# Performance work log

Hardware: AMD Instinct MI355X
Metric: run time of the kernel (lower is better)

The kernel has to match this reference:

```python
import jax, jax.numpy as jnp
import numpy as np

N = 100000
E = 1600000
H = 128
M = 256
L = 6
G = 512          # number of graphs in the batch
A = 95           # num_atom_types
EXTRA = 3        # input_dim - 1
EPS = 1e-5


def swish(x):
    return x * jax.nn.sigmoid(x)


def setup_inputs() -> dict:
    key = jax.random.key(0)
    ks = jax.random.split(key, 16)
    z = jax.random.randint(ks[0], (N, 1), 0, A).astype(jnp.float32)
    extra = jax.random.normal(ks[1], (N, EXTRA), dtype=jnp.float32)
    x = jnp.concatenate([z, extra], axis=1)                     # [N, 4]
    edge_index = jax.random.randint(ks[2], (2, E), 0, N)        # [2, E]
    batch = jnp.sort(jax.random.randint(ks[3], (N,), 0, G))     # [N]
    s = 0.02
    z_embed = jax.random.normal(ks[4], (A, H), dtype=jnp.float32) * s
    extra_w = jax.random.normal(ks[5], (H, EXTRA), dtype=jnp.float32) * (1.0 / np.sqrt(EXTRA))
    extra_b = jnp.zeros((H,), jnp.float32)
    conv_w = jax.random.normal(ks[6], (L, H, H), dtype=jnp.float32) * (1.0 / np.sqrt(H))
    conv_b = jnp.zeros((L, H), jnp.float32)
    gamma = jnp.ones((L, H), jnp.float32)
    beta = jnp.zeros((L, H), jnp.float32)
    mean_scale = jnp.ones((L, H), jnp.float32)
    mlp_w1 = jax.random.normal(ks[7], (L, M, H), dtype=jnp.float32) * (1.0 / np.sqrt(H))
    mlp_b1 = jnp.zeros((L, M), jnp.float32)
    mlp_w2 = jax.random.normal(ks[8], (L, H, M), dtype=jnp.float32) * (1.0 / np.sqrt(M))
    mlp_b2 = jnp.zeros((L, H), jnp.float32)
    return dict(x=x, edge_index=edge_index, batch=batch, z_embed=z_embed,
                extra_w=extra_w, extra_b=extra_b, conv_w=conv_w, conv_b=conv_b,
                gamma=gamma, beta=beta, mean_scale=mean_scale,
                mlp_w1=mlp_w1, mlp_b1=mlp_b1, mlp_w2=mlp_w2, mlp_b2=mlp_b2)


def gnn_forward(x, edge_index, batch, z_embed, extra_w, extra_b, conv_w, conv_b,
                gamma, beta, mean_scale, mlp_w1, mlp_b1, mlp_w2, mlp_b2):
    z = x[:, 0].astype(jnp.int32)
    h = z_embed[z] + x[:, 1:] @ extra_w.T + extra_b                 # [N, H]

    # GCN: add self loops, symmetric normalization (computed once; graph is static)
    loop = jnp.arange(N)
    src = jnp.concatenate([edge_index[0], loop])
    dst = jnp.concatenate([edge_index[1], loop])
    deg = jax.ops.segment_sum(jnp.ones_like(dst, jnp.float32), dst, num_segments=N)
    dinv = jnp.where(deg > 0, jax.lax.rsqrt(jnp.maximum(deg, 1.0)), 0.0)
    norm = (dinv[src] * dinv[dst])[:, None]                         # [E+N, 1]

    cnt = jax.ops.segment_sum(jnp.ones((N,), jnp.float32), batch, num_segments=G)[:, None]
    cnt = jnp.maximum(cnt, 1.0)

    for i in range(L):
        h_res = h
        # GCNConv
        xw = h @ conv_w[i].T
        agg = jax.ops.segment_sum(xw[src] * norm, dst, num_segments=N) + conv_b[i]
        # GraphNorm: gamma * (x - alpha*mean) / sqrt(var + eps) + beta, per graph
        mean = jax.ops.segment_sum(agg, batch, num_segments=G) / cnt   # [G, H]
        sub = agg - mean_scale[i] * mean[batch]
        var = jax.ops.segment_sum(sub * sub, batch, num_segments=G) / cnt
        hn = gamma[i] * sub * jax.lax.rsqrt(var[batch] + EPS) + beta[i]
        ha = swish(hn)
        # residual MLP
        h = swish(swish(ha @ mlp_w1[i].T + mlp_b1[i]) @ mlp_w2[i].T + mlp_b2[i]) + h_res
    return h


def reference(x, edge_index, batch, z_embed, extra_w, extra_b, conv_w, conv_b,
              gamma, beta, mean_scale, mlp_w1, mlp_b1, mlp_w2, mlp_b2):
    return gnn_forward(x, edge_index, batch, z_embed, extra_w, extra_b, conv_w, conv_b,
                       gamma, beta, mean_scale, mlp_w1, mlp_b1, mlp_w2, mlp_b2)
```

## Files before the change

kernel.cpp:

```cpp
#include <hip/hip_runtime.h>

#define NN 100000
#define EE 1600000
#define HH 128
#define MM 256
#define LL 6
#define GG 512
#define SCAN_NB ((NN + 1023) / 1024)

typedef __attribute__((ext_vector_type(8))) short short8;
typedef __attribute__((ext_vector_type(4))) float floatx4;

__device__ __forceinline__ float swishf(float v) {
    return v / (1.0f + __expf(-v));
}

__device__ __forceinline__ unsigned short f2bf(float f) {
    unsigned u = __builtin_bit_cast(unsigned, f);
    unsigned r = u + 0x7FFFu + ((u >> 16) & 1u);
    return (unsigned short)(r >> 16);
}

__device__ __forceinline__ float bf2f(unsigned short u) {
    return __builtin_bit_cast(float, (unsigned)u << 16);
}

__device__ __forceinline__ float2 bf2f2(unsigned u) {
    float2 r;
    r.x = __builtin_bit_cast(float, u << 16);
    r.y = __builtin_bit_cast(float, u & 0xFFFF0000u);
    return r;
}

__device__ __forceinline__ uint4 pack8(const float* o) {
    uint4 pk;
    pk.x = (unsigned)f2bf(o[0]) | ((unsigned)f2bf(o[1]) << 16);
    pk.y = (unsigned)f2bf(o[2]) | ((unsigned)f2bf(o[3]) << 16);
    pk.z = (unsigned)f2bf(o[4]) | ((unsigned)f2bf(o[5]) << 16);
    pk.w = (unsigned)f2bf(o[6]) | ((unsigned)f2bf(o[7]) << 16);
    return pk;
}

__global__ void k_embed(const float* __restrict__ x, const float* __restrict__ z_embed,
                        const float* __restrict__ ew, const float* __restrict__ eb,
                        unsigned short* __restrict__ hb) {
    int idx = blockIdx.x * blockDim.x + threadIdx.x;
    if (idx >= NN * 32) return;
    int n = idx >> 5;
    int c0 = (idx & 31) << 2;
    const float* xr = x + (size_t)n * 4;
    int z = (int)xr[0];
    float x1 = xr[1], x2 = xr[2], x3 = xr[3];
    const float* ze = z_embed + (size_t)z * HH + c0;
    float o[4];
#pragma unroll
    for (int j = 0; j < 4; ++j) {
        int c = c0 + j;
        o[j] = ze[j] + x1 * ew[c * 3 + 0] + x2 * ew[c * 3 + 1] + x3 * ew[c * 3 + 2] + eb[c];
    }
    uint2 p;
    p.x = (unsigned)f2bf(o[0]) | ((unsigned)f2bf(o[1]) << 16);
    p.y = (unsigned)f2bf(o[2]) | ((unsigned)f2bf(o[3]) << 16);
    *(uint2*)(hb + (size_t)n * HH + c0) = p;
}

__global__ void k_f2bf3(const float* __restrict__ s1, unsigned short* __restrict__ d1, int n1,
                        const float* __restrict__ s2, unsigned short* __restrict__ d2, int n2,
                        const float* __restrict__ s3, unsigned short* __restrict__ d3, int n3) {
    int i = blockIdx.x * blockDim.x + threadIdx.x;
    if (i < n1) {
        d1[i] = f2bf(s1[i]);
    } else if (i < n1 + n2) {
        d2[i - n1] = f2bf(s2[i - n1]);
    } else if (i < n1 + n2 + n3) {
        d3[i - n1 - n2] = f2bf(s3[i - n1 - n2]);
    }
}

__global__ __launch_bounds__(256) void k_degree_p(const int* __restrict__ dst,
                                                  int* __restrict__ deg) {
    int part = blockIdx.x & 7;
    int blk = blockIdx.x >> 3;
    int nb = gridDim.x >> 3;
    int lo = (int)((long long)part * NN / 8);
    int hi = (int)((long long)(part + 1) * NN / 8);
    for (int e = blk * 256 + threadIdx.x; e < EE; e += nb * 256) {
        int d = dst[e];
        if (d >= lo && d < hi) atomicAdd(&deg[d], 1);
    }
}

__global__ void k_dinv(const int* __restrict__ deg, float* __restrict__ dinv) {
    int n = blockIdx.x * blockDim.x + threadIdx.x;
    if (n < NN) dinv[n] = rsqrtf((float)(deg[n] + 1));
}

__global__ void k_scan1(const int* __restrict__ deg, int* __restrict__ bsum) {
    __shared__ int sd[256];
    int t = threadIdx.x;
    int base = blockIdx.x * 1024 + t * 4;
    int s = 0;
#pragma unroll
    for (int j = 0; j < 4; ++j) {
        int i = base + j;
        if (i < NN) s += deg[i];
    }
    sd[t] = s;
    __syncthreads();
    for (int off = 128; off > 0; off >>= 1) {
        if (t < off) sd[t] += sd[t + off];
        __syncthreads();
    }
    if (t == 0) bsum[blockIdx.x] = sd[0];
}

__global__ void k_scan2(const int* __restrict__ bsum, int* __restrict__ boff) {
    __shared__ int sd[128];
    int t = threadIdx.x;
    int v = (t < SCAN_NB) ? bsum[t] : 0;
    sd[t] = v;
    __syncthreads();
    for (int off = 1; off < 128; off <<= 1) {
        int u = (t >= off) ? sd[t - off] : 0;
        __syncthreads();
        sd[t] += u;
        __syncthreads();
    }
    boff[t] = sd[t] - v;
}

__global__ void k_scan3(const int* __restrict__ deg, const int* __restrict__ boff,
                        int* __restrict__ rowptr) {
    __shared__ int sd[256];
    int t = threadIdx.x;
    int base = blockIdx.x * 1024 + t * 4;
    int v[4];
    int s = 0;
#pragma unroll
    for (int j = 0; j < 4; ++j) {
        int i = base + j;
        v[j] = (i < NN) ? deg[i] : 0;
        s += v[j];
    }
    sd[t] = s;
    __syncthreads();
    for (int off = 1; off < 256; off <<= 1) {
        int u = (t >= off) ? sd[t - off] : 0;
        __syncthreads();
        sd[t] += u;
        __syncthreads();
    }
    int run = boff[blockIdx.x] + sd[t] - s;
#pragma unroll
    for (int j = 0; j < 4; ++j) {
        int i = base + j;
        if (i < NN) rowptr[i] = run;
        if (i == NN - 1) rowptr[NN] = run + v[j];
        run += v[j];
    }
}

__global__ __launch_bounds__(256) void k_fill_p(const int* __restrict__ ei,
                                                const int* __restrict__ rowptr,
                                                int* __restrict__ cursor,
                                                int* __restrict__ col) {
    int part = blockIdx.x & 7;
    int blk = blockIdx.x >> 3;
    int nb = gridDim.x >> 3;
    int lo = (int)((long long)part * NN / 8);
    int hi = (int)((long long)(part + 1) * NN / 8);
    for (int e = blk * 256 + threadIdx.x; e < EE; e += nb * 256) {
        int d = ei[EE + e];
        if (d >= lo && d < hi) {
            int p = atomicAdd(&cursor[d], 1);
            col[rowptr[d] + p] = ei[e];
        }
    }
}

__global__ void k_gptr(const int* __restrict__ batch, int* __restrict__ gptr) {
    int n = blockIdx.x * blockDim.x + threadIdx.x;
    if (n >= NN) return;
    int b = batch[n];
    int pb = (n == 0) ? -1 : batch[n - 1];
    for (int g = pb + 1; g <= b; ++g) gptr[g] = n;
    if (n == NN - 1) {
        for (int g = b + 1; g <= GG; ++g) gptr[g] = NN;
    }
}

__global__ __launch_bounds__(256) void k_conv(const unsigned short* __restrict__ A,
                                              const unsigned short* __restrict__ B,
                                              const float* __restrict__ dinv,
                                              unsigned short* __restrict__ Cb) {
    __shared__ unsigned short Bs[128][HH + 8];
    const int tid = threadIdx.x;
    const int wave = tid >> 6;
    const int lane = tid & 63;
    const int quad = lane >> 4;
    const int l16 = lane & 15;
    const int wr = (wave & 1) << 6;
    const int wc = (wave >> 1) << 6;
    const int rowBase = blockIdx.x * 128;

    for (int i = tid; i < 128 * (HH / 8); i += 256) {
        int r = i / (HH / 8);
        int kk = (i % (HH / 8)) * 8;
        int rho = (r & 64) | ((r & 3) << 4) | ((r >> 2) & 15);
        *(uint4*)(&Bs[rho][kk]) = *(const uint4*)(B + (size_t)r * HH + kk);
    }

    floatx4 acc[4][4];
    const floatx4 zed = {0.f, 0.f, 0.f, 0.f};
#pragma unroll
    for (int i = 0; i < 4; ++i)
#pragma unroll
        for (int j = 0; j < 4; ++j) acc[i][j] = zed;

    int ar[4];
#pragma unroll
    for (int i = 0; i < 4; ++i) {
        int r = rowBase + wr + (i << 4) + l16;
        ar[i] = r < NN ? r : NN - 1;
    }

    __syncthreads();

#pragma unroll
    for (int ks = 0; ks < HH / 32; ++ks) {
        int k = (ks << 5) + (quad << 3);
        short8 a[4], b[4];
#pragma unroll
        for (int i = 0; i < 4; ++i) a[i] = *(const short8*)(A + (size_t)ar[i] * HH + k);
#pragma unroll
        for (int j = 0; j < 4; ++j) b[j] = *(const short8*)(&Bs[wc + (j << 4) + l16][k]);
#pragma unroll
        for (int i = 0; i < 4; ++i)
#pragma unroll
            for (int j = 0; j < 4; ++j)
                acc[i][j] =
                    __builtin_amdgcn_mfma_f32_16x16x32_bf16(a[i], b[j], acc[i][j], 0, 0, 0);
    }

    const int c0 = wc + (l16 << 2);
#pragma unroll
    for (int i = 0; i < 4; ++i) {
        int rb = rowBase + wr + (i << 4) + (quad << 2);
#pragma unroll
        for (int reg = 0; reg < 4; ++reg) {
            int r = rb + reg;
            if (r < NN) {
                float dv = dinv[r];
                float o[4];
#pragma unroll
                for (int j = 0; j < 4; ++j) o[j] = acc[i][j][reg] * dv;
                uint2 pk;
                pk.x = (unsigned)f2bf(o[0]) | ((unsigned)f2bf(o[1]) << 16);
                pk.y = (unsigned)f2bf(o[2]) | ((unsigned)f2bf(o[3]) << 16);
                *(uint2*)(Cb + (size_t)r * HH + c0) = pk;
            }
        }
    }
}

__global__ __launch_bounds__(256) void k_mlp(const unsigned short* __restrict__ ha,
                                             const unsigned short* __restrict__ W1,
                                             const float* __restrict__ b1,
                                             const unsigned short* __restrict__ W2,
                                             const float* __restrict__ b2,
                                             unsigned short* __restrict__ hb,
                                             float* __restrict__ h_out, int writeF) {
    __shared__ unsigned short ts[64][MM + 8];
    const int tid = threadIdx.x;
    const int wave = tid >> 6;
    const int lane = tid & 63;
    const int quad = lane >> 4;
    const int l16 = lane & 15;
    const int wrh = (wave & 1) << 5;
    const int rowBase = blockIdx.x * 64;

    const int wch = (wave >> 1) << 7;
    floatx4 acc1[2][8];
    const floatx4 zed = {0.f, 0.f, 0.f, 0.f};
#pragma unroll
    for (int i = 0; i < 2; ++i)
#pragma unroll
        for (int j = 0; j < 8; ++j) acc1[i][j] = zed;

    int ar[2];
#pragma unroll
    for (int i = 0; i < 2; ++i) {
        int r = rowBase + wrh + (i << 4) + l16;
        ar[i] = r < NN ? r : NN - 1;
    }

#pragma unroll
    for (int ks = 0; ks < HH / 32; ++ks) {
        int k = (ks << 5) + (quad << 3);
        short8 a[2], b[8];
#pragma unroll
        for (int i = 0; i < 2; ++i) a[i] = *(const short8*)(ha + (size_t)ar[i] * HH + k);
#pragma unroll
        for (int j = 0; j < 8; ++j) {
            int pc = wch + (l16 << 3) + j;
            b[j] = *(const short8*)(W1 + (size_t)pc * HH + k);
        }
#pragma unroll
        for (int i = 0; i < 2; ++i)
#pragma unroll
            for (int j = 0; j < 8; ++j)
                acc1[i][j] =
                    __builtin_amdgcn_mfma_f32_16x16x32_bf16(a[i], b[j], acc1[i][j], 0, 0, 0);
    }

    const int c0a = wch + (l16 << 3);
    float b1v[8];
    {
        float4 u = *(const float4*)(b1 + c0a);
        float4 v = *(const float4*)(b1 + c0a + 4);
        b1v[0] = u.x; b1v[1] = u.y; b1v[2] = u.z; b1v[3] = u.w;
        b1v[4] = v.x; b1v[5] = v.y; b1v[6] = v.z; b1v[7] = v.w;
    }
#pragma unroll
    for (int i = 0; i < 2; ++i) {
#pragma unroll
        for (int reg = 0; reg < 4; ++reg) {
            int lr = wrh + (i << 4) + (quad << 2) + reg;
            float o[8];
#pragma unroll
            for (int j = 0; j < 8; ++j) o[j] = swishf(acc1[i][j][reg] + b1v[j]);
            *(uint4*)(&ts[lr][c0a]) = pack8(o);
        }
    }
    __syncthreads();

    const int wc2 = (wave >> 1) << 6;
    floatx4 acc2[2][4];
#pragma unroll
    for (int i = 0; i < 2; ++i)
#pragma unroll
        for (int j = 0; j < 4; ++j) acc2[i][j] = zed;

#pragma unroll
    for (int ks = 0; ks < MM / 32; ++ks) {
        int k = (ks << 5) + (quad << 3);
        short8 a[2], b[4];
#pragma unroll
        for (int i = 0; i < 2; ++i)
            a[i] = *(const short8*)(&ts[wrh + (i << 4) + l16][k]);
#pragma unroll
        for (int j = 0; j < 4; ++j) {
            int pc = wc2 + (l16 << 2) + j;
            b[j] = *(const short8*)(W2 + (size_t)pc * MM + k);
        }
#pragma unroll
        for (int i = 0; i < 2; ++i)
#pragma unroll
            for (int j = 0; j < 4; ++j)
                acc2[i][j] =
                    __builtin_amdgcn_mfma_f32_16x16x32_bf16(a[i], b[j], acc2[i][j], 0, 0, 0);
    }

    const int c0 = wc2 + (l16 << 2);
    float4 b2v = *(const float4*)(b2 + c0);
    float bv[4] = {b2v.x, b2v.y, b2v.z, b2v.w};
#pragma unroll
    for (int i = 0; i < 2; ++i) {
        int rb = rowBase + wrh + (i << 4) + (quad << 2);
#pragma unroll
        for (int reg = 0; reg < 4; ++reg) {
            int r = rb + reg;
            if (r < NN) {
                uint2 rv = *(const uint2*)(hb + (size_t)r * HH + c0);
                float2 r01 = bf2f2(rv.x), r23 = bf2f2(rv.y);
                float o[4];
                o[0] = swishf(acc2[i][0][reg] + bv[0]) + r01.x;
                o[1] = swishf(acc2[i][1][reg] + bv[1]) + r01.y;
                o[2] = swishf(acc2[i][2][reg] + bv[2]) + r23.x;
                o[3] = swishf(acc2[i][3][reg] + bv[3]) + r23.y;
                uint2 pk;
                pk.x = (unsigned)f2bf(o[0]) | ((unsigned)f2bf(o[1]) << 16);
                pk.y = (unsigned)f2bf(o[2]) | ((unsigned)f2bf(o[3]) << 16);
                *(uint2*)(hb + (size_t)r * HH + c0) = pk;
                if (writeF)
                    *(float4*)(h_out + (size_t)r * HH + c0) =
                        make_float4(o[0], o[1], o[2], o[3]);
            }
        }
    }
}

__global__ __launch_bounds__(256) void k_agg(const unsigned short* __restrict__ y,
                                             const int* __restrict__ rowptr,
                                             const int* __restrict__ col,
                                             const float* __restrict__ dinv,
                                             const float* __restrict__ cb,
                                             unsigned short* __restrict__ agg) {
    int w = threadIdx.x >> 6;
    int lane = threadIdx.x & 63;
    int d = blockIdx.x * 4 + w;
    if (d >= NN) return;
    int grp = lane >> 4;
    int l16 = lane & 15;
    const uint4* yv = (const uint4*)y;
    float acc[8];
#pragma unroll
    for (int j = 0; j < 8; ++j) acc[j] = 0.f;
    if (grp == 0) {
        uint4 v = yv[(size_t)d * 16 + l16];
        float2 p0 = bf2f2(v.x), p1 = bf2f2(v.y), p2 = bf2f2(v.z), p3 = bf2f2(v.w);
        acc[0] = p0.x; acc[1] = p0.y; acc[2] = p1.x; acc[3] = p1.y;
        acc[4] = p2.x; acc[5] = p2.y; acc[6] = p3.x; acc[7] = p3.y;
    }
    int beg = rowptr[d];
    int end = rowptr[d + 1];
    for (int e = beg + grp; e < end; e += 4) {
        int s = col[e];
        uint4 v = yv[(size_t)s * 16 + l16];
        float2 p0 = bf2f2(v.x), p1 = bf2f2(v.y), p2 = bf2f2(v.z), p3 = bf2f2(v.w);
        acc[0] += p0.x; acc[1] += p0.y; acc[2] += p1.x; acc[3] += p1.y;
        acc[4] += p2.x; acc[5] += p2.y; acc[6] += p3.x; acc[7] += p3.y;
    }
#pragma unroll
    for (int j = 0; j < 8; ++j) {
        acc[j] += __shfl_xor(acc[j], 16, 64);
        acc[j] += __shfl_xor(acc[j], 32, 64);
    }
    if (grp == 0) {
        float dv = dinv[d];
        float4 c0 = *(const float4*)(cb + l16 * 8);
        float4 c1 = *(const float4*)(cb + l16 * 8 + 4);
        float o[8];
        o[0] = acc[0] * dv + c0.x; o[1] = acc[1] * dv + c0.y;
        o[2] = acc[2] * dv + c0.z; o[3] = acc[3] * dv + c0.w;
        o[4] = acc[4] * dv + c1.x; o[5] = acc[5] * dv + c1.y;
        o[6] = acc[6] * dv + c1.z; o[7] = acc[7] * dv + c1.w;
        *(uint4*)(agg + (size_t)d * HH + l16 * 8) = pack8(o);
    }
}

__global__ __launch_bounds__(512) void k_stats(const unsigned short* __restrict__ agg,
                                               const int* __restrict__ gptr,
                                               const float* __restrict__ ms,
                                               float* __restrict__ gmean,
                                               float* __restrict__ grstd) {
    __shared__ float s1[512];
    __shared__ float s2[512];
    int g = blockIdx.x;
    int t = threadIdx.x;
    int c = t & 127;
    int part = t >> 7;
    int beg = gptr[g];
    int end = gptr[g + 1];
    float S1 = 0.f, S2 = 0.f;
    for (int n = beg + part; n < end; n += 4) {
        float v = bf2f(agg[(size_t)n * HH + c]);
        S1 += v;
        S2 += v * v;
    }
    s1[t] = S1;
    s2[t] = S2;
    __syncthreads();
    if (part == 0) {
        S1 = (s1[c] + s1[c + 128]) + (s1[c + 256] + s1[c + 384]);
        S2 = (s2[c] + s2[c + 128]) + (s2[c + 256] + s2[c + 384]);
        int cnt = end - beg;
        float inv = 1.0f / (float)(cnt > 0 ? cnt : 1);
        float m = S1 * inv;
        float msc = ms[c];
        float var = S2 * inv - msc * (2.0f - msc) * m * m;
        gmean[g * HH + c] = m;
        grstd[g * HH + c] = rsqrtf(var + 1e-5f);
    }
}

__global__ void k_normswish(const unsigned short* __restrict__ agg,
                            const int* __restrict__ batch, const float* __restrict__ gamma,
                            const float* __restrict__ beta, const float* __restrict__ ms,
                            const float* __restrict__ gmean, const float* __restrict__ grstd,
                            unsigned short* __restrict__ ha) {
    int idx = blockIdx.x * blockDim.x + threadIdx.x;
    if (idx >= NN * 32) return;
    int n = idx >> 5;
    int c0 = (idx & 31) << 2;
    int g = batch[n];
    uint2 ain = *(const uint2*)(agg + (size_t)n * HH + c0);
    float2 a01 = bf2f2(ain.x);
    float2 a23 = bf2f2(ain.y);
    float av[4] = {a01.x, a01.y, a23.x, a23.y};
    unsigned short o[4];
#pragma unroll
    for (int j = 0; j < 4; ++j) {
        int c = c0 + j;
        float sub = av[j] - ms[c] * gmean[g * HH + c];
        float hn = gamma[c] * sub * grstd[g * HH + c] + beta[c];
        o[j] = f2bf(swishf(hn));
    }
    uint2 p;
    p.x = (unsigned)o[0] | ((unsigned)o[1] << 16);
    p.y = (unsigned)o[2] | ((unsigned)o[3] << 16);
    *(uint2*)(ha + (size_t)n * HH + c0) = p;
}

extern "C" void kernel_launch(void* const* d_in, const int* in_sizes, int n_in,
                              void* d_out, int out_size, void* d_ws, size_t ws_size,
                              hipStream_t stream) {
    const float* x = (const float*)d_in[0];
    const int* ei = (const int*)d_in[1];
    const int* batch = (const int*)d_in[2];
    const float* z_embed = (const float*)d_in[3];
    const float* extra_w = (const float*)d_in[4];
    const float* extra_b = (const float*)d_in[5];
    const float* conv_w = (const float*)d_in[6];
    const float* conv_b = (const float*)d_in[7];
    const float* gamma = (const float*)d_in[8];
    const float* beta = (const float*)d_in[9];
    const float* mean_scale = (const float*)d_in[10];
    const float* mlp_w1 = (const float*)d_in[11];
    const float* mlp_b1 = (const float*)d_in[12];
    const float* mlp_w2 = (const float*)d_in[13];
    const float* mlp_b2 = (const float*)d_in[14];
    float* h_out = (float*)d_out;

    char* wsB = (char*)d_ws;
    size_t off = 0;
    auto alloc = [&](size_t bytes) -> void* {
        void* p = (void*)(wsB + off);
        off = (off + bytes + 255) & ~(size_t)255;
        return p;
    };
    float* dinv = (float*)alloc((size_t)NN * 4);
    int* deg = (int*)alloc((size_t)NN * 4);
    int* cursor = (int*)alloc((size_t)NN * 4);
    int* rowptr = (int*)alloc((size_t)(NN + 1) * 4);
    int* bsum = (int*)alloc(128 * 4);
    int* boff = (int*)alloc(128 * 4);
    int* col = (int*)alloc((size_t)EE * 4);
    int* gptr = (int*)alloc((size_t)(GG + 1) * 4);
    float* gmean = (float*)alloc((size_t)GG * HH * 4);
    float* grstd = (float*)alloc((size_t)GG * HH * 4);
    unsigned short* wb =
        (unsigned short*)alloc((size_t)(LL * (HH * HH + MM * HH + HH * MM)) * 2);
    unsigned short* cwb = wb;
    unsigned short* w1b = wb + (size_t)LL * HH * HH;
    unsigned short* w2b = w1b + (size_t)LL * MM * HH;
    unsigned short* hb = (unsigned short*)alloc((size_t)NN * HH * 2);
    unsigned short* ybuf = (unsigned short*)alloc((size_t)NN * HH * 2);
    unsigned short* aggb = (unsigned short*)alloc((size_t)NN * HH * 2);

    hipMemsetAsync(deg, 0, (size_t)NN * 4, stream);
    hipMemsetAsync(cursor, 0, (size_t)NN * 4, stream);

    k_embed<<<(NN * 32 + 255) / 256, 256, 0, stream>>>(x, z_embed, extra_w, extra_b, hb);
    {
        int n1 = LL * HH * HH, n2 = LL * MM * HH, n3 = LL * HH * MM;
        int nt = n1 + n2 + n3;
        k_f2bf3<<<(nt + 255) / 256, 256, 0, stream>>>(conv_w, cwb, n1, mlp_w1, w1b, n2,
                                                      mlp_w2, w2b, n3);
    }
    k_degree_p<<<1024, 256, 0, stream>>>(ei + EE, deg);
    k_dinv<<<(NN + 255) / 256, 256, 0, stream>>>(deg, dinv);
    k_scan1<<<SCAN_NB, 256, 0, stream>>>(deg, bsum);
    k_scan2<<<1, 128, 0, stream>>>(bsum, boff);
    k_scan3<<<SCAN_NB, 256, 0, stream>>>(deg, boff, rowptr);
    k_fill_p<<<1024, 256, 0, stream>>>(ei, rowptr, cursor, col);
    k_gptr<<<(NN + 255) / 256, 256, 0, stream>>>(batch, gptr);

    int gconv = (NN + 127) / 128;
    int gmlp = (NN + 63) / 64;
    for (int i = 0; i < LL; ++i) {
        k_conv<<<gconv, 256, 0, stream>>>(hb, cwb + (size_t)i * HH * HH, dinv, ybuf);
        k_agg<<<(NN + 3) / 4, 256, 0, stream>>>(ybuf, rowptr, col, dinv,
                                                conv_b + (size_t)i * HH, aggb);
        k_stats<<<GG, 512, 0, stream>>>(aggb, gptr, mean_scale + (size_t)i * HH, gmean, grstd);
        k_normswish<<<(NN * 32 + 255) / 256, 256, 0, stream>>>(
            aggb, batch, gamma + (size_t)i * HH, beta + (size_t)i * HH,
            mean_scale + (size_t)i * HH, gmean, grstd, ybuf);
        k_mlp<<<gmlp, 256, 0, stream>>>(ybuf, w1b + (size_t)i * MM * HH,
                                        mlp_b1 + (size_t)i * MM, w2b + (size_t)i * HH * MM,
                                        mlp_b2 + (size_t)i * HH, hb, h_out,
                                        i == LL - 1 ? 1 : 0);
    }
}
```

Before: 1.445 ms.

## Fuse GraphNorm-swish, residual MLP and next-layer conv GEMM into one kernel

The per-layer normswish, MLP and next layer's conv GEMM kernels are merged into a single kernel. k_stats now precomputes per-graph affine coefficients (scale and shift) so normalization becomes one FMA applied while loading the A operand. The MLP output is staged in shared memory and immediately multiplied by the next layer's conv weights, which avoids writing and re-reading the normalized activations and the hidden state in global memory. In exchange the fused kernel holds more registers and LDS, which may reduce occupancy, and the conv GEMM now uses 64-row tiles instead of 128.

Result: faster. 1.416 ms (-2.0%).

```diff
diff --git a/kernel.cpp b/kernel.cpp
--- a/kernel.cpp
+++ b/kernel.cpp
@@ -32,12 +32,25 @@
     return r;
 }
 
+__device__ __forceinline__ void unpack8(uint4 v, float* a) {
+    float2 p0 = bf2f2(v.x), p1 = bf2f2(v.y), p2 = bf2f2(v.z), p3 = bf2f2(v.w);
+    a[0] = p0.x; a[1] = p0.y; a[2] = p1.x; a[3] = p1.y;
+    a[4] = p2.x; a[5] = p2.y; a[6] = p3.x; a[7] = p3.y;
+}
+
 __device__ __forceinline__ uint4 pack8(const float* o) {
     uint4 pk;
     pk.x = (unsigned)f2bf(o[0]) | ((unsigned)f2bf(o[1]) << 16);
     pk.y = (unsigned)f2bf(o[2]) | ((unsigned)f2bf(o[3]) << 16);
     pk.z = (unsigned)f2bf(o[4]) | ((unsigned)f2bf(o[5]) << 16);
     pk.w = (unsigned)f2bf(o[6]) | ((unsigned)f2bf(o[7]) << 16);
+    return pk;
+}
+
+__device__ __forceinline__ uint2 pack4(const float* o) {
+    uint2 pk;
+    pk.x = (unsigned)f2bf(o[0]) | ((unsigned)f2bf(o[1]) << 16);
+    pk.y = (unsigned)f2bf(o[2]) | ((unsigned)f2bf(o[3]) << 16);
     return pk;
 }
 
@@ -58,10 +71,7 @@
         int c = c0 + j;
         o[j] = ze[j] + x1 * ew[c * 3 + 0] + x2 * ew[c * 3 + 1] + x3 * ew[c * 3 + 2] + eb[c];
     }
-    uint2 p;
-    p.x = (unsigned)f2bf(o[0]) | ((unsigned)f2bf(o[1]) << 16);
-    p.y = (unsigned)f2bf(o[2]) | ((unsigned)f2bf(o[3]) << 16);
-    *(uint2*)(hb + (size_t)n * HH + c0) = p;
+    *(uint2*)(hb + (size_t)n * HH + c0) = pack4(o);
 }
 
 __global__ void k_f2bf3(const float* __restrict__ s1, unsigned short* __restrict__ d1, int n1,
@@ -254,137 +264,7 @@
                 float o[4];
 #pragma unroll
                 for (int j = 0; j < 4; ++j) o[j] = acc[i][j][reg] * dv;
-                uint2 pk;
-                pk.x = (unsigned)f2bf(o[0]) | ((unsigned)f2bf(o[1]) << 16);
-                pk.y = (unsigned)f2bf(o[2]) | ((unsigned)f2bf(o[3]) << 16);
-                *(uint2*)(Cb + (size_t)r * HH + c0) = pk;
-            }
-        }
-    }
-}
-
-__global__ __launch_bounds__(256) void k_mlp(const unsigned short* __restrict__ ha,
-                                             const unsigned short* __restrict__ W1,
-                                             const float* __restrict__ b1,
-                                             const unsigned short* __restrict__ W2,
-                                             const float* __restrict__ b2,
-                                             unsigned short* __restrict__ hb,
-                                             float* __restrict__ h_out, int writeF) {
-    __shared__ unsigned short ts[64][MM + 8];
-    const int tid = threadIdx.x;
-    const int wave = tid >> 6;
-    const int lane = tid & 63;
-    const int quad = lane >> 4;
-    const int l16 = lane & 15;
-    const int wrh = (wave & 1) << 5;
-    const int rowBase = blockIdx.x * 64;
-
-    const int wch = (wave >> 1) << 7;
-    floatx4 acc1[2][8];
-    const floatx4 zed = {0.f, 0.f, 0.f, 0.f};
-#pragma unroll
-    for (int i = 0; i < 2; ++i)
-#pragma unroll
-        for (int j = 0; j < 8; ++j) acc1[i][j] = zed;
-
-    int ar[2];
-#pragma unroll
-    for (int i = 0; i < 2; ++i) {
-        int r = rowBase + wrh + (i << 4) + l16;
-        ar[i] = r < NN ? r : NN - 1;
-    }
-
-#pragma unroll
-    for (int ks = 0; ks < HH / 32; ++ks) {
-        int k = (ks << 5) + (quad << 3);
-        short8 a[2], b[8];
-#pragma unroll
-        for (int i = 0; i < 2; ++i) a[i] = *(const short8*)(ha + (size_t)ar[i] * HH + k);
-#pragma unroll
-        for (int j = 0; j < 8; ++j) {
-            int pc = wch + (l16 << 3) + j;
-            b[j] = *(const short8*)(W1 + (size_t)pc * HH + k);
-        }
-#pragma unroll
-        for (int i = 0; i < 2; ++i)
-#pragma unroll
-            for (int j = 0; j < 8; ++j)
-                acc1[i][j] =
-                    __builtin_amdgcn_mfma_f32_16x16x32_bf16(a[i], b[j], acc1[i][j], 0, 0, 0);
-    }
-
-    const int c0a = wch + (l16 << 3);
-    float b1v[8];
-    {
-        float4 u = *(const float4*)(b1 + c0a);
-        float4 v = *(const float4*)(b1 + c0a + 4);
-        b1v[0] = u.x; b1v[1] = u.y; b1v[2] = u.z; b1v[3] = u.w;
-        b1v[4] = v.x; b1v[5] = v.y; b1v[6] = v.z; b1v[7] = v.w;
-    }
-#pragma unroll
-    for (int i = 0; i < 2; ++i) {
-#pragma unroll
-        for (int reg = 0; reg < 4; ++reg) {
-            int lr = wrh + (i << 4) + (quad << 2) + reg;
-            float o[8];
-#pragma unroll
-            for (int j = 0; j < 8; ++j) o[j] = swishf(acc1[i][j][reg] + b1v[j]);
-            *(uint4*)(&ts[lr][c0a]) = pack8(o);
-        }
-    }
-    __syncthreads();
-
-    const int wc2 = (wave >> 1) << 6;
-    floatx4 acc2[2][4];
-#pragma unroll
-    for (int i = 0; i < 2; ++i)
-#pragma unroll
-        for (int j = 0; j < 4; ++j) acc2[i][j] = zed;
-
-#pragma unroll
-    for (int ks = 0; ks < MM / 32; ++ks) {
-        int k = (ks << 5) + (quad << 3);
-        short8 a[2], b[4];
-#pragma unroll
-        for (int i = 0; i < 2; ++i)
-            a[i] = *(const short8*)(&ts[wrh + (i << 4) + l16][k]);
-#pragma unroll
-        for (int j = 0; j < 4; ++j) {
-            int pc = wc2 + (l16 << 2) + j;
-            b[j] = *(const short8*)(W2 + (size_t)pc * MM + k);
-        }
-#pragma unroll
-        for (int i = 0; i < 2; ++i)
-#pragma unroll
-            for (int j = 0; j < 4; ++j)
-                acc2[i][j] =
-                    __builtin_amdgcn_mfma_f32_16x16x32_bf16(a[i], b[j], acc2[i][j], 0, 0, 0);
-    }
-
-    const int c0 = wc2 + (l16 << 2);
-    float4 b2v = *(const float4*)(b2 + c0);
-    float bv[4] = {b2v.x, b2v.y, b2v.z, b2v.w};
-#pragma unroll
-    for (int i = 0; i < 2; ++i) {
-        int rb = rowBase + wrh + (i << 4) + (quad << 2);
-#pragma unroll
-        for (int reg = 0; reg < 4; ++reg) {
-            int r = rb + reg;
-            if (r < NN) {
-                uint2 rv = *(const uint2*)(hb + (size_t)r * HH + c0);
-                float2 r01 = bf2f2(rv.x), r23 = bf2f2(rv.y);
-                float o[4];
-                o[0] = swishf(acc2[i][0][reg] + bv[0]) + r01.x;
-                o[1] = swishf(acc2[i][1][reg] + bv[1]) + r01.y;
-                o[2] = swishf(acc2[i][2][reg] + bv[2]) + r23.x;
-                o[3] = swishf(acc2[i][3][reg] + bv[3]) + r23.y;
-                uint2 pk;
-                pk.x = (unsigned)f2bf(o[0]) | ((unsigned)f2bf(o[1]) << 16);
-                pk.y = (unsigned)f2bf(o[2]) | ((unsigned)f2bf(o[3]) << 16);
-                *(uint2*)(hb + (size_t)r * HH + c0) = pk;
-                if (writeF)
-                    *(float4*)(h_out + (size_t)r * HH + c0) =
-                        make_float4(o[0], o[1], o[2], o[3]);
+                *(uint2*)(Cb + (size_t)r * HH + c0) = pack4(o);
             }
         }
     }
@@ -408,18 +288,17 @@
     for (int j = 0; j < 8; ++j) acc[j] = 0.f;
     if (grp == 0) {
         uint4 v = yv[(size_t)d * 16 + l16];
-        float2 p0 = bf2f2(v.x), p1 = bf2f2(v.y), p2 = bf2f2(v.z), p3 = bf2f2(v.w);
-        acc[0] = p0.x; acc[1] = p0.y; acc[2] = p1.x; acc[3] = p1.y;
-        acc[4] = p2.x; acc[5] = p2.y; acc[6] = p3.x; acc[7] = p3.y;
+        unpack8(v, acc);
     }
     int beg = rowptr[d];
     int end = rowptr[d + 1];
     for (int e = beg + grp; e < end; e += 4) {
         int s = col[e];
         uint4 v = yv[(size_t)s * 16 + l16];
-        float2 p0 = bf2f2(v.x), p1 = bf2f2(v.y), p2 = bf2f2(v.z), p3 = bf2f2(v.w);
-        acc[0] += p0.x; acc[1] += p0.y; acc[2] += p1.x; acc[3] += p1.y;
-        acc[4] += p2.x; acc[5] += p2.y; acc[6] += p3.x; acc[7] += p3.y;
+        float b0[8];
+        unpack8(v, b0);
+#pragma unroll
+        for (int k = 0; k < 8; ++k) acc[k] += b0[k];
     }
 #pragma unroll
     for (int j = 0; j < 8; ++j) {
@@ -442,8 +321,10 @@
 __global__ __launch_bounds__(512) void k_stats(const unsigned short* __restrict__ agg,
                                                const int* __restrict__ gptr,
                                                const float* __restrict__ ms,
-                                               float* __restrict__ gmean,
-                                               float* __restrict__ grstd) {
+                                               const float* __restrict__ gamma,
+                                               const float* __restrict__ beta,
+                                               float* __restrict__ c1,
+                                               float* __restrict__ c0) {
     __shared__ float s1[512];
     __shared__ float s2[512];
     int g = blockIdx.x;
@@ -469,37 +350,210 @@
         float m = S1 * inv;
         float msc = ms[c];
         float var = S2 * inv - msc * (2.0f - msc) * m * m;
-        gmean[g * HH + c] = m;
-        grstd[g * HH + c] = rsqrtf(var + 1e-5f);
-    }
-}
-
-__global__ void k_normswish(const unsigned short* __restrict__ agg,
-                            const int* __restrict__ batch, const float* __restrict__ gamma,
-                            const float* __restrict__ beta, const float* __restrict__ ms,
-                            const float* __restrict__ gmean, const float* __restrict__ grstd,
-                            unsigned short* __restrict__ ha) {
-    int idx = blockIdx.x * blockDim.x + threadIdx.x;
-    if (idx >= NN * 32) return;
-    int n = idx >> 5;
-    int c0 = (idx & 31) << 2;
-    int g = batch[n];
-    uint2 ain = *(const uint2*)(agg + (size_t)n * HH + c0);
-    float2 a01 = bf2f2(ain.x);
-    float2 a23 = bf2f2(ain.y);
-    float av[4] = {a01.x, a01.y, a23.x, a23.y};
-    unsigned short o[4];
-#pragma unroll
-    for (int j = 0; j < 4; ++j) {
-        int c = c0 + j;
-        float sub = av[j] - ms[c] * gmean[g * HH + c];
-        float hn = gamma[c] * sub * grstd[g * HH + c] + beta[c];
-        o[j] = f2bf(swishf(hn));
-    }
-    uint2 p;
-    p.x = (unsigned)o[0] | ((unsigned)o[1] << 16);
-    p.y = (unsigned)o[2] | ((unsigned)o[3] << 16);
-    *(uint2*)(ha + (size_t)n * HH + c0) = p;
+        float rstd = rsqrtf(var + 1e-5f);
+        float c1v = gamma[c] * rstd;
+        c1[g * HH + c] = c1v;
+        c0[g * HH + c] = beta[c] - c1v * msc * m;
+    }
+}
+
+__global__ __launch_bounds__(256) void k_mega(const unsigned short* __restrict__ agg,
+                                              const int* __restrict__ batch,
+                                              const float* __restrict__ c1,
+                                              const float* __restrict__ c0,
+                                              const unsigned short* __restrict__ W1,
+                                              const float* __restrict__ b1,
+                                              const unsigned short* __restrict__ W2,
+                                              const float* __restrict__ b2,
+                                              const unsigned short* __restrict__ Wc,
+                                              const float* __restrict__ dinv,
+                                              unsigned short* __restrict__ hb,
+                                              float* __restrict__ h_out,
+                                              unsigned short* __restrict__ y_out, int writeF,
+                                              int doConv) {
+    __shared__ unsigned short smem[64 * (MM + 8)];
+    const int tid = threadIdx.x;
+    const int wave = tid >> 6;
+    const int lane = tid & 63;
+    const int quad = lane >> 4;
+    const int l16 = lane & 15;
+    const int wrh = (wave & 1) << 5;
+    const int wch = (wave >> 1) << 7;
+    const int wc2 = (wave >> 1) << 6;
+    const int rowBase = blockIdx.x * 64;
+    const floatx4 zed = {0.f, 0.f, 0.f, 0.f};
+
+    int ar[2], gi[2];
+#pragma unroll
+    for (int i = 0; i < 2; ++i) {
+        int r = rowBase + wrh + (i << 4) + l16;
+        ar[i] = r < NN ? r : NN - 1;
+        gi[i] = batch[ar[i]];
+    }
+
+    short8 a_all[4][2];
+#pragma unroll
+    for (int ks = 0; ks < 4; ++ks) {
+        int k = (ks << 5) + (quad << 3);
+#pragma unroll
+        for (int i = 0; i < 2; ++i) {
+            uint4 raw = *(const uint4*)(agg + (size_t)ar[i] * HH + k);
+            float v[8];
+            unpack8(raw, v);
+            const float* c1p = c1 + gi[i] * HH + k;
+            const float* c0p = c0 + gi[i] * HH + k;
+            float4 c1a = *(const float4*)c1p;
+            float4 c1b = *(const float4*)(c1p + 4);
+            float4 c0a = *(const float4*)c0p;
+            float4 c0b = *(const float4*)(c0p + 4);
+            float cc1[8] = {c1a.x, c1a.y, c1a.z, c1a.w, c1b.x, c1b.y, c1b.z, c1b.w};
+            float cc0[8] = {c0a.x, c0a.y, c0a.z, c0a.w, c0b.x, c0b.y, c0b.z, c0b.w};
+            short8 av;
+#pragma unroll
+            for (int j = 0; j < 8; ++j)
+                av[j] = (short)f2bf(swishf(cc1[j] * v[j] + cc0[j]));
+            a_all[ks][i] = av;
+        }
+    }
+
+    const int c0a = wch + (l16 << 3);
+#pragma unroll
+    for (int jh = 0; jh < 2; ++jh) {
+        floatx4 acc1[2][4];
+#pragma unroll
+        for (int i = 0; i < 2; ++i)
+#pragma unroll
+            for (int j = 0; j < 4; ++j) acc1[i][j] = zed;
+#pragma unroll
+        for (int ks = 0; ks < 4; ++ks) {
+            int k = (ks << 5) + (quad << 3);
+            short8 b[4];
+#pragma unroll
+            for (int j = 0; j < 4; ++j) {
+                int pc = c0a + (jh << 2) + j;
+                b[j] = *(const short8*)(W1 + (size_t)pc * HH + k);
+            }
+#pragma unroll
+            for (int i = 0; i < 2; ++i)
+#pragma unroll
+                for (int j = 0; j < 4; ++j)
+                    acc1[i][j] = __builtin_amdgcn_mfma_f32_16x16x32_bf16(a_all[ks][i], b[j],
+                                                                         acc1[i][j], 0, 0, 0);
+        }
+        float4 b4 = *(const float4*)(b1 + c0a + (jh << 2));
+        float bv[4] = {b4.x, b4.y, b4.z, b4.w};
+#pragma unroll
+        for (int i = 0; i < 2; ++i) {
+#pragma unroll
+            for (int reg = 0; reg < 4; ++reg) {
+                int lr = wrh + (i << 4) + (quad << 2) + reg;
+                float o[4];
+#pragma unroll
+                for (int j = 0; j < 4; ++j) o[j] = swishf(acc1[i][j][reg] + bv[j]);
+                *(uint2*)(&smem[lr * (MM + 8) + c0a + (jh << 2)]) = pack4(o);
+            }
+        }
+    }
+    __syncthreads();
+
+    floatx4 acc2[2][4];
+#pragma unroll
+    for (int i = 0; i < 2; ++i)
+#pragma unroll
+        for (int j = 0; j < 4; ++j) acc2[i][j] = zed;
+#pragma unroll
+    for (int ks = 0; ks < MM / 32; ++ks) {
+        int k = (ks << 5) + (quad << 3);
+        short8 a[2], b[4];
+#pragma unroll
+        for (int i = 0; i < 2; ++i)
+            a[i] = *(const short8*)(&smem[(wrh + (i << 4) + l16) * (MM + 8) + k]);
+#pragma unroll
+        for (int j = 0; j < 4; ++j) {
+            int pc = wc2 + (l16 << 2) + j;
+            b[j] = *(const short8*)(W2 + (size_t)pc * MM + k);
+        }
+#pragma unroll
+        for (int i = 0; i < 2; ++i)
+#pragma unroll
+            for (int j = 0; j < 4; ++j)
+                acc2[i][j] =
+                    __builtin_amdgcn_mfma_f32_16x16x32_bf16(a[i], b[j], acc2[i][j], 0, 0, 0);
+    }
+    __syncthreads();
+
+    const int co = wc2 + (l16 << 2);
+    {
+        float4 b4 = *(const float4*)(b2 + co);
+        float bv[4] = {b4.x, b4.y, b4.z, b4.w};
+#pragma unroll
+        for (int i = 0; i < 2; ++i) {
+            int rb = rowBase + wrh + (i << 4) + (quad << 2);
+#pragma unroll
+            for (int reg = 0; reg < 4; ++reg) {
+                int r = rb + reg;
+                if (r < NN) {
+                    uint2 rv = *(const uint2*)(hb + (size_t)r * HH + co);
+                    float2 r01 = bf2f2(rv.x), r23 = bf2f2(rv.y);
+                    float o[4];
+                    o[0] = swishf(acc2[i][0][reg] + bv[0]) + r01.x;
+                    o[1] = swishf(acc2[i][1][reg] + bv[1]) + r01.y;
+                    o[2] = swishf(acc2[i][2][reg] + bv[2]) + r23.x;
+                    o[3] = swishf(acc2[i][3][reg] + bv[3]) + r23.y;
+                    uint2 pk = pack4(o);
+                    *(uint2*)(hb + (size_t)r * HH + co) = pk;
+                    if (writeF)
+                        *(float4*)(h_out + (size_t)r * HH + co) =
+                            make_float4(o[0], o[1], o[2], o[3]);
+                    int lr = wrh + (i << 4) + (quad << 2) + reg;
+                    *(uint2*)(&smem[lr * 136 + co]) = pk;
+                }
+            }
+        }
+    }
+
+    if (doConv) {
+        __syncthreads();
+        floatx4 acc3[2][4];
+#pragma unroll
+        for (int i = 0; i < 2; ++i)
+#pragma unroll
+            for (int j = 0; j < 4; ++j) acc3[i][j] = zed;
+#pragma unroll
+        for (int ks = 0; ks < 4; ++ks) {
+            int k = (ks << 5) + (quad << 3);
+            short8 a[2], b[4];
+#pragma unroll
+            for (int i = 0; i < 2; ++i)
+                a[i] = *(const short8*)(&smem[(wrh + (i << 4) + l16) * 136 + k]);
+#pragma unroll
+            for (int j = 0; j < 4; ++j) {
+                int pc = wc2 + (l16 << 2) + j;
+                b[j] = *(const short8*)(Wc + (size_t)pc * HH + k);
+            }
+#pragma unroll
+            for (int i = 0; i < 2; ++i)
+#pragma unroll
+                for (int j = 0; j < 4; ++j)
+                    acc3[i][j] =
+                        __builtin_amdgcn_mfma_f32_16x16x32_bf16(a[i], b[j], acc3[i][j], 0, 0, 0);
+        }
+#pragma unroll
+        for (int i = 0; i < 2; ++i) {
+            int rb = rowBase + wrh + (i << 4) + (quad << 2);
+#pragma unroll
+            for (int reg = 0; reg < 4; ++reg) {
+                int r = rb + reg;
+                if (r < NN) {
+                    float dv = dinv[r];
+                    float o[4];
+#pragma unroll
+                    for (int j = 0; j < 4; ++j) o[j] = acc3[i][j][reg] * dv;
+                    *(uint2*)(y_out + (size_t)r * HH + co) = pack4(o);
+                }
+            }
+        }
+    }
 }
 
 extern "C" void kernel_launch(void* const* d_in, const int* in_sizes, int n_in,
@@ -537,8 +591,8 @@
     int* boff = (int*)alloc(128 * 4);
     int* col = (int*)alloc((size_t)EE * 4);
     int* gptr = (int*)alloc((size_t)(GG + 1) * 4);
-    float* gmean = (float*)alloc((size_t)GG * HH * 4);
-    float* grstd = (float*)alloc((size_t)GG * HH * 4);
+    float* c1t = (float*)alloc((size_t)GG * HH * 4);
+    float* c0t = (float*)alloc((size_t)GG * HH * 4);
     unsigned short* wb =
         (unsigned short*)alloc((size_t)(LL * (HH * HH + MM * HH + HH * MM)) * 2);
     unsigned short* cwb = wb;
@@ -567,18 +621,18 @@
     k_gptr<<<(NN + 255) / 256, 256, 0, stream>>>(batch, gptr);
 
     int gconv = (NN + 127) / 128;
-    int gmlp = (NN + 63) / 64;
+    int gmega = (NN + 63) / 64;
+    k_conv<<<gconv, 256, 0, stream>>>(hb, cwb, dinv, ybuf);
     for (int i = 0; i < LL; ++i) {
-        k_conv<<<gconv, 256, 0, stream>>>(hb, cwb + (size_t)i * HH * HH, dinv, ybuf);
         k_agg<<<(NN + 3) / 4, 256, 0, stream>>>(ybuf, rowptr, col, dinv,
                                                 conv_b + (size_t)i * HH, aggb);
-        k_stats<<<GG, 512, 0, stream>>>(aggb, gptr, mean_scale + (size_t)i * HH, gmean, grstd);
-        k_normswish<<<(NN * 32 + 255) / 256, 256, 0, stream>>>(
-            aggb, batch, gamma + (size_t)i * HH, beta + (size_t)i * HH,
-            mean_scale + (size_t)i * HH, gmean, grstd, ybuf);
-        k_mlp<<<gmlp, 256, 0, stream>>>(ybuf, w1b + (size_t)i * MM * HH,
-                                        mlp_b1 + (size_t)i * MM, w2b + (size_t)i * HH * MM,
-                                        mlp_b2 + (size_t)i * HH, hb, h_out,
-                                        i == LL - 1 ? 1 : 0);
-    }
-}
+        k_stats<<<GG, 512, 0, stream>>>(aggb, gptr, mean_scale + (size_t)i * HH,
+                                        gamma + (size_t)i * HH, beta + (size_t)i * HH, c1t,
+                                        c0t);
+        k_mega<<<gmega, 256, 0, stream>>>(
+            aggb, batch, c1t, c0t, w1b + (size_t)i * MM * HH, mlp_b1 + (size_t)i * MM,
+            w2b + (size_t)i * HH * MM, mlp_b2 + (size_t)i * HH,
+            cwb + (size_t)(i + 1 < LL ? i + 1 : 0) * HH * HH, dinv, hb, h_out, ybuf,
+            i == LL - 1 ? 1 : 0, i < LL - 1 ? 1 : 0);
+    }
+}
```
